# Kernel optimization log

Measured on AMD Instinct MI355X. Metric: run time of the kernel, lower is better.

Reference implementation:

```python
import jax, jax.numpy as jnp
import numpy as np

N, F, H, E, ES, G = 50000, 64, 4, 300000, 400000, 128
NS, EPS = 0.2, 1e-5  # LeakyReLU slope, BN eps


def setup_inputs() -> dict:
    k = jax.random.split(jax.random.key(0), 16)
    rn = lambda i, s, sc=1.0: jax.random.normal(k[i], s, jnp.float32) * sc
    return {
        "x": rn(0, (N, F)),
        "edge_index": jax.random.randint(k[1], (2, E), 0, N),
        "batch": jnp.sort(jax.random.randint(k[2], (N,), 0, G)),
        "scatter_edge_index": jax.random.randint(k[3], (4, 2, ES), 0, N),
        "scatter_edge_attr": rn(4, (4, ES), 0.1),
        "gat_W": rn(5, (4, F, H * F), 0.05),
        "gat_asrc": rn(6, (4, H, F), 0.05),
        "gat_adst": rn(7, (4, H, F), 0.05),
        "gat_bias": jnp.zeros((4, H * F)),
        "mlp_W": rn(8, (4, H * F, F), 0.05),
        "mlp_b": jnp.zeros((4, F)),
        "mlp_g": jnp.ones((4, F)), "mlp_beta": jnp.zeros((4, F)),
        "mlp_rm": jnp.zeros((4, F)), "mlp_rv": jax.random.uniform(k[9], (4, F)) + 0.5,
        "fc1_W": rn(10, (F, 256), 0.05), "fc1_b": jnp.zeros((256,)),
        "fc1_g": jnp.ones((256,)), "fc1_beta": jnp.zeros((256,)),
        "fc1_rm": jnp.zeros((256,)), "fc1_rv": jax.random.uniform(k[11], (256,)) + 0.5,
        "fc2_W": rn(12, (256, 64), 0.05), "fc2_b": jnp.zeros((64,)),
        "fc2_g": jnp.ones((64,)), "fc2_beta": jnp.zeros((64,)),
        "fc2_rm": jnp.zeros((64,)), "fc2_rv": jax.random.uniform(k[13], (64,)) + 0.5,
        "fc3_W": rn(14, (64, 10), 0.05), "fc3_b": jnp.zeros((10,)),
        "fc3_g": jnp.ones((10,)), "fc3_beta": jnp.zeros((10,)),
        "fc3_rm": jnp.zeros((10,)), "fc3_rv": jax.random.uniform(k[15], (10,)) + 0.5,
    }


def _bn(h, g, b, rm, rv):
    # BatchNorm1d in eval mode (running stats)
    return g * (h - rm) * jax.lax.rsqrt(rv + EPS) + b


def _forward(floats, ints):
    (x, sea, gW, gas, gad, gb, mW, mb, mg, mbe, mrm, mrv,
     f1W, f1b, f1g, f1be, f1rm, f1rv, f2W, f2b, f2g, f2be, f2rm, f2rv,
     f3W, f3b, f3g, f3be, f3rm, f3rv) = floats
    edge_index, batch, sei = ints
    n = x.shape[0]
    loop = jnp.arange(n)
    src = jnp.concatenate([edge_index[0], loop])  # GATConv adds self-loops
    dst = jnp.concatenate([edge_index[1], loop])

    def solo(i, h):
        # edge_attr-weighted scatter-add (solo_pass, aggr='add')
        s, t = sei[i, 0], sei[i, 1]
        return jax.ops.segment_sum(sea[i][:, None] * h[s], t, num_segments=n)

    def gat_mlp(i, h):
        hh = (h @ gW[i]).reshape(n, H, F)                       # [N,H,F]
        e = (hh * gas[i]).sum(-1)[src] + (hh * gad[i]).sum(-1)[dst]  # [E+N,H]
        e = jnp.where(e > 0, e, NS * e)                         # LeakyReLU(0.2)
        m = jax.ops.segment_max(e, dst, num_segments=n)         # segment softmax over dst
        ex = jnp.exp(e - m[dst])
        ssum = jax.ops.segment_sum(ex, dst, num_segments=n)
        alpha = ex / ssum[dst]
        out = jax.ops.segment_sum(hh[src] * alpha[:, :, None], dst, num_segments=n)
        out = out.reshape(n, H * F) + gb[i]                     # concat heads + bias
        h2 = jax.nn.elu(out) @ mW[i] + mb[i]                    # ELU -> Dropout(eval) -> Linear
        return _bn(h2, mg[i], mbe[i], mrm[i], mrv[i])

    x0 = solo(0, x)
    xh = [jnp.abs(solo(i, x)) for i in (1, 2, 3)]
    branches = [x0] + [solo(0, h) for h in xh]
    branches = [gat_mlp(i, branches[i]) for i in range(4)]
    x_stage2 = x + branches[0] + branches[1] + branches[2] + branches[3]
    pooled = jax.ops.segment_sum(x_stage2, batch, num_segments=G)   # global_add_pool
    h = jax.nn.relu(_bn(pooled @ f1W + f1b, f1g, f1be, f1rm, f1rv))
    h = jax.nn.relu(_bn(h @ f2W + f2b, f2g, f2be, f2rm, f2rv))
    return _bn(h @ f3W + f3b, f3g, f3be, f3rm, f3rv)  # [G, num_classes]


def reference(x, edge_index, batch, scatter_edge_index, scatter_edge_attr, gat_W, gat_asrc, gat_adst, gat_bias, mlp_W, mlp_b, mlp_g, mlp_beta, mlp_rm, mlp_rv, fc1_W, fc1_b, fc1_g, fc1_beta, fc1_rm, fc1_rv, fc2_W, fc2_b, fc2_g, fc2_beta, fc2_rm, fc2_rv, fc3_W, fc3_b, fc3_g, fc3_beta, fc3_rm, fc3_rv):
    floats = (x, scatter_edge_attr, gat_W, gat_asrc, gat_adst, gat_bias, mlp_W, mlp_b, mlp_g, mlp_beta, mlp_rm, mlp_rv, fc1_W, fc1_b, fc1_g, fc1_beta, fc1_rm, fc1_rv, fc2_W, fc2_b, fc2_g, fc2_beta, fc2_rm, fc2_rv, fc3_W, fc3_b, fc3_g, fc3_beta, fc3_rm, fc3_rv)
    return _forward(floats, (edge_index, batch, scatter_edge_index))
```

## Files before the change

kernel.cpp:

```cpp
#include <hip/hip_runtime.h>

typedef unsigned int uint;
typedef unsigned short u16;

#define NN 50000
#define FF 64
#define NHD 4
#define EE 300000
#define ESN 400000
#define NG 128
#define NSLOPE 0.2f
#define EPSBN 1e-5f

#define BINSZ 64
#define NBIN 782
#define CHUNK 2048
#define NBLK 196
#define BST 40
#define BCAP 38

typedef float f32x4 __attribute__((ext_vector_type(4)));
typedef float f32x2 __attribute__((ext_vector_type(2)));
typedef short bf16x8 __attribute__((ext_vector_type(8)));
union U8 { uint4 u; bf16x8 s; };

static __device__ __forceinline__ float lrelu(float e) {
  return fmaxf(e, NSLOPE * e);
}
static __device__ __forceinline__ float bl(uint u) {
  return __uint_as_float(u << 16);
}
static __device__ __forceinline__ float bh(uint u) {
  return __uint_as_float(u & 0xFFFF0000u);
}
static __device__ __forceinline__ uint f2bf(float f) {
  uint u = __float_as_uint(f);
  return (u + 0x7FFFu + ((u >> 16) & 1u)) >> 16;
}
static __device__ __forceinline__ uint packbf(float a, float b) {
  return f2bf(a) | (f2bf(b) << 16);
}

__global__ __launch_bounds__(256) void k_setup(
    const float2* __restrict__ x, const float* __restrict__ gW,
    const float* __restrict__ gas, const float* __restrict__ gad,
    const float* __restrict__ mW, const float* __restrict__ mb,
    const float* __restrict__ mg, const float* __restrict__ mbe,
    const float* __restrict__ mrm, const float* __restrict__ mrv,
    uint* __restrict__ xbf, uint* __restrict__ WB2, float* __restrict__ wasd,
    uint* __restrict__ MB, float* __restrict__ cvec) {
  int i = blockIdx.x * 256 + threadIdx.x;
  if (i < NN * 32) {
    float2 v = x[i];
    xbf[i] = packbf(v.x, v.y);
  }
  int t = i;
  if (t < 8192) {
    int b = t >> 11, id = t & 2047;
    int h = id >> 9, r2 = id & 511;
    int q2 = r2 >> 8, r3 = r2 & 255;
    int ct = r3 >> 6, l = r3 & 63;
    int c = h * 64 + ct * 16 + (l & 15);
    int k0 = q2 * 32 + (l >> 4) * 8;
    const float* Wp = gW + b * 16384;
    uint4 o;
    o.x = packbf(Wp[(k0 + 0) * 256 + c], Wp[(k0 + 1) * 256 + c]);
    o.y = packbf(Wp[(k0 + 2) * 256 + c], Wp[(k0 + 3) * 256 + c]);
    o.z = packbf(Wp[(k0 + 4) * 256 + c], Wp[(k0 + 5) * 256 + c]);
    o.w = packbf(Wp[(k0 + 6) * 256 + c], Wp[(k0 + 7) * 256 + c]);
    ((uint4*)WB2)[t] = o;
  } else if (t < 8192 + 2048) {
    int id = t - 8192;
    int b = id >> 9, r = id & 511;
    int sd = r >> 8, r2 = r & 255;
    int h = r2 >> 6, k = r2 & 63;
    const float* Wp = gW + b * 16384;
    const float* ap = (sd ? gad : gas) + b * 256 + h * 64;
    float acc = 0.f;
    for (int f = 0; f < 64; ++f) acc += Wp[k * 256 + h * 64 + f] * ap[f];
    wasd[((b * 2 + sd) * 4 + h) * 64 + k] = acc;
  } else if (t < 8192 + 2048 + 8192) {
    int id = t - 10240;
    int b = id >> 11, rem = id & 2047;
    int tt = rem >> 6, l = rem & 63;
    int tile = tt >> 3, q2 = tt & 7;
    int c = tile * 16 + (l & 15);
    int k0 = q2 * 32 + (l >> 4) * 8;
    const float* Mp = mW + b * 16384;
    float sc = mg[b * 64 + c] * rsqrtf(mrv[b * 64 + c] + EPSBN);
    float v[8];
#pragma unroll
    for (int j = 0; j < 8; ++j) v[j] = Mp[(k0 + j) * 64 + c] * sc;
    uint4 o;
    o.x = packbf(v[0], v[1]); o.y = packbf(v[2], v[3]);
    o.z = packbf(v[4], v[5]); o.w = packbf(v[6], v[7]);
    ((uint4*)MB)[id] = o;
  } else if (t < 8192 + 2048 + 8192 + 64) {
    int c = t - 18432;
    float acc = 0.f;
#pragma unroll
    for (int b = 0; b < 4; ++b) {
      float sc = mg[b * 64 + c] * rsqrtf(mrv[b * 64 + c] + EPSBN);
      acc += sc * (mb[b * 64 + c] - mrm[b * 64 + c]) + mbe[b * 64 + c];
    }
    cvec[c] = acc;
  }
}

__global__ __launch_bounds__(256) void k_sort1(
    const int* __restrict__ sei, const float* __restrict__ sea,
    const int* __restrict__ ei, uint2* __restrict__ sorted,
    u16* __restrict__ offs) {
  __shared__ uint hist[NBIN];
  __shared__ uint wsum[4];
  __shared__ __align__(16) uint2 buf[CHUNK];
  int y = blockIdx.y, blk = blockIdx.x, tid = threadIdx.x;
  int E = (y < 4) ? ESN : EE;
  int e0 = blk * CHUNK;
  if (e0 >= E) return;
  int ec = E - e0; if (ec > CHUNK) ec = CHUNK;
  for (int i = tid; i < NBIN; i += 256) hist[i] = 0;
  __syncthreads();
  const int* sptr; const int* tptr; const float* wptr = 0;
  if (y < 4) {
    sptr = sei + (size_t)y * 2 * ESN; tptr = sptr + ESN;
    wptr = sea + (size_t)y * ESN;
  } else {
    sptr = ei; tptr = ei + EE;
  }
  uint2 rec[8]; uint rbin[8];
#pragma unroll
  for (int k = 0; k < 8; ++k) {
    int idx = tid + k * 256;
    rbin[k] = 0xFFFFFFFFu;
    if (idx < ec) {
      int e = e0 + idx;
      int s = sptr[e], t = tptr[e];
      uint w = (y < 4) ? (f2bf(wptr[e]) << 16) : 0u;
      rec[k].x = (uint)s | ((uint)(t & 63) << 16);
      rec[k].y = w;
      rbin[k] = (uint)(t >> 6);
      atomicAdd(&hist[rbin[k]], 1u);
    }
  }
  __syncthreads();
  int t4 = tid * 4;
  uint h0 = 0, h1 = 0, h2 = 0, h3 = 0;
  if (t4 + 0 < NBIN) h0 = hist[t4 + 0];
  if (t4 + 1 < NBIN) h1 = hist[t4 + 1];
  if (t4 + 2 < NBIN) h2 = hist[t4 + 2];
  if (t4 + 3 < NBIN) h3 = hist[t4 + 3];
  uint sl = h0 + h1 + h2 + h3;
  uint pre = sl;
#pragma unroll
  for (int off = 1; off < 64; off <<= 1) {
    uint nv = __shfl_up(pre, off);
    if ((tid & 63) >= off) pre += nv;
  }
  int wid = tid >> 6;
  if ((tid & 63) == 63) wsum[wid] = pre;
  __syncthreads();
  uint wbase = 0;
#pragma unroll
  for (int w = 0; w < 4; ++w) if (w < wid) wbase += wsum[w];
  uint base = wbase + pre - sl;
  if (t4 + 0 < NBIN) hist[t4 + 0] = base;
  if (t4 + 1 < NBIN) hist[t4 + 1] = base + h0;
  if (t4 + 2 < NBIN) hist[t4 + 2] = base + h0 + h1;
  if (t4 + 3 < NBIN) hist[t4 + 3] = base + h0 + h1 + h2;
  __syncthreads();
  u16* ob = offs + ((size_t)y * NBLK + blk) * 784;
  for (int i = tid; i < NBIN; i += 256) ob[i] = (u16)hist[i];
  if (tid == 0) { ob[NBIN] = (u16)ec; ob[NBIN + 1] = (u16)ec; }
  __syncthreads();
#pragma unroll
  for (int k = 0; k < 8; ++k) {
    if (rbin[k] != 0xFFFFFFFFu) {
      uint p = atomicAdd(&hist[rbin[k]], 1u);
      buf[p] = rec[k];
    }
  }
  __syncthreads();
  uint2* sb = sorted + ((size_t)y * NBLK + blk) * CHUNK;
  uint4* s4 = (uint4*)sb;
  const uint4* b4 = (const uint4*)buf;
  int n4 = (ec + 1) >> 1;
  for (int i = tid; i < n4; i += 256) s4[i] = b4[i];
}

__global__ __launch_bounds__(256) void k_sort2(
    const u16* __restrict__ offs, const uint2* __restrict__ sorted,
    uint* __restrict__ pbk, uint* __restrict__ gbk) {
  __shared__ __align__(16) uint Lb[BINSZ * BST];
  __shared__ uint Lc[BINSZ];
  int y = blockIdx.y, bin = blockIdx.x, tid = threadIdx.x;
  if (tid < BINSZ) Lc[tid] = 0u;
  __syncthreads();
  int nblk = (y < 4) ? NBLK : 147;
  for (int sb = tid; sb < nblk; sb += 256) {
    const u16* ob = offs + ((size_t)y * NBLK + sb) * 784;
    uint st = ob[bin], en = ob[bin + 1];
    const uint2* src = sorted + ((size_t)y * NBLK + sb) * CHUNK;
    for (uint i = st; i < en; ++i) {
      uint2 r = src[i];
      uint tl = (r.x >> 16) & 63u;
      uint p = atomicAdd(&Lc[tl], 1u);
      if (p < BCAP) Lb[tl * BST + 2 + p] = (r.x & 0xFFFFu) | r.y;
    }
  }
  __syncthreads();
  if (tid < BINSZ) Lb[tid * BST] = Lc[tid];
  __syncthreads();
  int n0 = bin * BINSZ;
  int nodes = NN - n0;
  if (nodes > BINSZ) nodes = BINSZ;
  uint* out = (y < 4) ? (pbk + ((size_t)y * NN + n0) * BST)
                      : (gbk + (size_t)n0 * BST);
  int tot4 = nodes * (BST / 4);
  uint4* o4v = (uint4*)out;
  const uint4* L4 = (const uint4*)Lb;
  for (int i = tid; i < tot4; i += 256) o4v[i] = L4[i];
}

__global__ __launch_bounds__(256) void k_solo_gA(
    const uint* __restrict__ xbf, const uint* __restrict__ pbk,
    const float* __restrict__ wasd, uint* __restrict__ bbuf,
    uint* __restrict__ tmpb, float* __restrict__ es4,
    float* __restrict__ ed4) {
  int i = blockIdx.y;
  int tid = threadIdx.x;
  int n = blockIdx.x * 32 + (tid >> 3);
  int sl = tid & 7;
  if (n >= NN) return;
  const uint* bk = pbk + ((size_t)i * NN + n) * BST;
  int deg = (int)bk[0]; deg = deg > BCAP ? BCAP : deg;
  const uint* pp = bk + 2;
  f32x2 A0 = {0.f, 0.f}, A1 = {0.f, 0.f}, A2 = {0.f, 0.f}, A3 = {0.f, 0.f};
  f32x2 B0 = {0.f, 0.f}, B1 = {0.f, 0.f}, B2 = {0.f, 0.f}, B3 = {0.f, 0.f};
  for (int j = 0; j < deg; j += 2) {
    uint2 pe2 = *(const uint2*)&pp[j];
    if (j + 1 >= deg) pe2.y = 0u;
    float w0 = bh(pe2.x), w1 = bh(pe2.y);
    f32x2 w20 = {w0, w0}, w21 = {w1, w1};
    uint4 v0 = *(const uint4*)&xbf[(size_t)(pe2.x & 0xFFFFu) * 32 + sl * 4];
    uint4 v1 = *(const uint4*)&xbf[(size_t)(pe2.y & 0xFFFFu) * 32 + sl * 4];
    A0 += (f32x2){bl(v0.x), bh(v0.x)} * w20;
    A1 += (f32x2){bl(v0.y), bh(v0.y)} * w20;
    A2 += (f32x2){bl(v0.z), bh(v0.z)} * w20;
    A3 += (f32x2){bl(v0.w), bh(v0.w)} * w20;
    B0 += (f32x2){bl(v1.x), bh(v1.x)} * w21;
    B1 += (f32x2){bl(v1.y), bh(v1.y)} * w21;
    B2 += (f32x2){bl(v1.z), bh(v1.z)} * w21;
    B3 += (f32x2){bl(v1.w), bh(v1.w)} * w21;
  }
  A0 += B0; A1 += B1; A2 += B2; A3 += B3;
  uint4 o;
  o.x = packbf(A0[0], A0[1]); o.y = packbf(A1[0], A1[1]);
  o.z = packbf(A2[0], A2[1]); o.w = packbf(A3[0], A3[1]);
  uint* out = (i == 0) ? bbuf : (tmpb + (size_t)(i - 1) * NN * 32);
  *(uint4*)&out[(size_t)n * 32 + sl * 4] = o;
  if (i == 0) {
    float pv[8] = {A0[0], A0[1], A1[0], A1[1], A2[0], A2[1], A3[0], A3[1]};
    const float* wa = wasd;
    float r[8];
#pragma unroll
    for (int o8 = 0; o8 < 8; ++o8) {
      const float* w8 = wa + o8 * 64 + sl * 8;
      float a = 0.f;
#pragma unroll
      for (int j = 0; j < 8; ++j) a += pv[j] * w8[j];
      r[o8] = a;
    }
#pragma unroll
    for (int off = 1; off < 8; off <<= 1)
#pragma unroll
      for (int o8 = 0; o8 < 8; ++o8) r[o8] += __shfl_xor(r[o8], off);
    if (sl == 0) {
      *(float4*)&es4[(size_t)n * 4] = make_float4(r[0], r[1], r[2], r[3]);
      *(float4*)&ed4[(size_t)n * 4] = make_float4(r[4], r[5], r[6], r[7]);
    }
  }
}

__global__ __launch_bounds__(256) void k_solo_gB(
    const uint* __restrict__ tmpb, const uint* __restrict__ pbk,
    const float* __restrict__ wasd, uint* __restrict__ bbuf,
    float* __restrict__ es4, float* __restrict__ ed4) {
  int j0 = blockIdx.y;
  int b = j0 + 1;
  int tid = threadIdx.x;
  int n = blockIdx.x * 32 + (tid >> 3);
  int sl = tid & 7;
  if (n >= NN) return;
  const uint* bk = pbk + (size_t)n * BST;
  int deg = (int)bk[0]; deg = deg > BCAP ? BCAP : deg;
  const uint* pp = bk + 2;
  const uint* tin = tmpb + (size_t)j0 * NN * 32;
  f32x2 A0 = {0.f, 0.f}, A1 = {0.f, 0.f}, A2 = {0.f, 0.f}, A3 = {0.f, 0.f};
  f32x2 B0 = {0.f, 0.f}, B1 = {0.f, 0.f}, B2 = {0.f, 0.f}, B3 = {0.f, 0.f};
  for (int j = 0; j < deg; j += 2) {
    uint2 pe2 = *(const uint2*)&pp[j];
    if (j + 1 >= deg) pe2.y = 0u;
    float w0 = bh(pe2.x), w1 = bh(pe2.y);
    f32x2 w20 = {w0, w0}, w21 = {w1, w1};
    uint4 v0 = *(const uint4*)&tin[(size_t)(pe2.x & 0xFFFFu) * 32 + sl * 4];
    uint4 v1 = *(const uint4*)&tin[(size_t)(pe2.y & 0xFFFFu) * 32 + sl * 4];
    A0 += (f32x2){fabsf(bl(v0.x)), fabsf(bh(v0.x))} * w20;
    A1 += (f32x2){fabsf(bl(v0.y)), fabsf(bh(v0.y))} * w20;
    A2 += (f32x2){fabsf(bl(v0.z)), fabsf(bh(v0.z))} * w20;
    A3 += (f32x2){fabsf(bl(v0.w)), fabsf(bh(v0.w))} * w20;
    B0 += (f32x2){fabsf(bl(v1.x)), fabsf(bh(v1.x))} * w21;
    B1 += (f32x2){fabsf(bl(v1.y)), fabsf(bh(v1.y))} * w21;
    B2 += (f32x2){fabsf(bl(v1.z)), fabsf(bh(v1.z))} * w21;
    B3 += (f32x2){fabsf(bl(v1.w)), fabsf(bh(v1.w))} * w21;
  }
  A0 += B0; A1 += B1; A2 += B2; A3 += B3;
  uint4 o;
  o.x = packbf(A0[0], A0[1]); o.y = packbf(A1[0], A1[1]);
  o.z = packbf(A2[0], A2[1]); o.w = packbf(A3[0], A3[1]);
  *(uint4*)&bbuf[(size_t)b * NN * 32 + (size_t)n * 32 + sl * 4] = o;
  {
    float pv[8] = {A0[0], A0[1], A1[0], A1[1], A2[0], A2[1], A3[0], A3[1]};
    const float* wa = wasd + b * 512;
    float r[8];
#pragma unroll
    for (int o8 = 0; o8 < 8; ++o8) {
      const float* w8 = wa + o8 * 64 + sl * 8;
      float a = 0.f;
#pragma unroll
      for (int j = 0; j < 8; ++j) a += pv[j] * w8[j];
      r[o8] = a;
    }
#pragma unroll
    for (int off = 1; off < 8; off <<= 1)
#pragma unroll
      for (int o8 = 0; o8 < 8; ++o8) r[o8] += __shfl_xor(r[o8], off);
    if (sl == 0) {
      *(float4*)&es4[(size_t)b * NN * 4 + (size_t)n * 4] =
          make_float4(r[0], r[1], r[2], r[3]);
      *(float4*)&ed4[(size_t)b * NN * 4 + (size_t)n * 4] =
          make_float4(r[4], r[5], r[6], r[7]);
    }
  }
}

__global__ __launch_bounds__(256) void k_agg(
    const uint* __restrict__ gbk, const float* __restrict__ es4,
    const float* __restrict__ ed4, const uint* __restrict__ bbuf,
    uint* __restrict__ agg4) {
  __shared__ uint gbr[32][40];
  __shared__ uint2 meta[32][32];
  int br = blockIdx.y;
  const float4* es44 = (const float4*)(es4 + (size_t)br * NN * 4);
  const float4* ed44 = (const float4*)(ed4 + (size_t)br * NN * 4);
  const uint* bbf = bbuf + (size_t)br * NN * 32;
  int tid = threadIdx.x;
  int n0 = blockIdx.x * 32;
  for (int idx = tid; idx < 320; idx += 256) {
    int i = idx / 10, q = idx % 10;
    int nd = n0 + i;
    uint4 v = (nd < NN) ? *(const uint4*)&gbk[(size_t)nd * BST + q * 4]
                        : make_uint4(0, 0, 0, 0);
    *(uint4*)&gbr[i][q * 4] = v;
  }
  __syncthreads();
  {
    int g = tid >> 5, hl = tid & 31;
#pragma unroll
    for (int rep = 0; rep < 4; ++rep) {
      int i = rep * 8 + g;
      int nd = n0 + i;
      bool vld = nd < NN;
      int nds = vld ? nd : 0;
      int deg = vld ? (int)gbr[i][0] : 0;
      deg = deg > 31 ? 31 : deg;
      int s0 = (hl < deg) ? (int)gbr[i][2 + hl] : nds;
      bool act = hl <= deg;
      float4 edd = ed44[nds];
      float4 e4 = es44[s0];
      float val[4];
      val[0] = act ? lrelu(e4.x + edd.x) : -3e38f;
      val[1] = act ? lrelu(e4.y + edd.y) : -3e38f;
      val[2] = act ? lrelu(e4.z + edd.z) : -3e38f;
      val[3] = act ? lrelu(e4.w + edd.w) : -3e38f;
      float m[4] = {val[0], val[1], val[2], val[3]};
#pragma unroll
      for (int off = 1; off < 32; off <<= 1)
#pragma unroll
        for (int h = 0; h < 4; ++h) m[h] = fmaxf(m[h], __shfl_xor(m[h], off));
      float e[4], sm[4];
#pragma unroll
      for (int h = 0; h < 4; ++h) {
        e[h] = act ? __expf(val[h] - m[h]) : 0.f;
        sm[h] = e[h];
      }
#pragma unroll
      for (int off = 1; off < 32; off <<= 1)
#pragma unroll
        for (int h = 0; h < 4; ++h) sm[h] += __shfl_xor(sm[h], off);
      meta[i][hl] = make_uint2(packbf(e[0] / sm[0], e[1] / sm[1]),
                               packbf(e[2] / sm[2], e[3] / sm[3]));
    }
  }
  __syncthreads();
  {
    int wv = tid >> 6, l = tid & 63;
    int i = wv * 8 + (l >> 3), sl = l & 7;
    int nd = n0 + i;
    bool vld = nd < NN;
    int self = vld ? nd : 0;
    int deg = vld ? (int)gbr[i][0] : 0;
    deg = deg > 31 ? 31 : deg;
    int tot = deg + 1;
    f32x2 a00={0.f,0.f},a01={0.f,0.f},a02={0.f,0.f},a03={0.f,0.f};
    f32x2 a10={0.f,0.f},a11={0.f,0.f},a12={0.f,0.f},a13={0.f,0.f};
    f32x2 a20={0.f,0.f},a21={0.f,0.f},a22={0.f,0.f},a23={0.f,0.f};
    f32x2 a30={0.f,0.f},a31={0.f,0.f},a32={0.f,0.f},a33={0.f,0.f};
    f32x2 c00={0.f,0.f},c01={0.f,0.f},c02={0.f,0.f},c03={0.f,0.f};
    f32x2 c10={0.f,0.f},c11={0.f,0.f},c12={0.f,0.f},c13={0.f,0.f};
    f32x2 c20={0.f,0.f},c21={0.f,0.f},c22={0.f,0.f},c23={0.f,0.f};
    f32x2 c30={0.f,0.f},c31={0.f,0.f},c32={0.f,0.f},c33={0.f,0.f};
    for (int j = 0; j < tot; j += 2) {
      int j1 = j + 1;
      int src0 = (j < deg) ? (int)gbr[i][2 + j] : self;
      int src1 = (j1 < deg) ? (int)gbr[i][2 + j1] : self;
      uint2 al0 = meta[i][j];
      uint2 al1 = meta[i][j1];
      uint4 v0 = *(const uint4*)&bbf[(size_t)src0 * 32 + sl * 4];
      uint4 v1 = *(const uint4*)&bbf[(size_t)src1 * 32 + sl * 4];
      f32x2 w0={bl(al0.x),bl(al0.x)}, w1={bh(al0.x),bh(al0.x)};
      f32x2 w2={bl(al0.y),bl(al0.y)}, w3={bh(al0.y),bh(al0.y)};
      f32x2 p0={bl(v0.x),bh(v0.x)}, p1={bl(v0.y),bh(v0.y)};
      f32x2 p2={bl(v0.z),bh(v0.z)}, p3={bl(v0.w),bh(v0.w)};
      a00+=p0*w0; a01+=p1*w0; a02+=p2*w0; a03+=p3*w0;
      a10+=p0*w1; a11+=p1*w1; a12+=p2*w1; a13+=p3*w1;
      a20+=p0*w2; a21+=p1*w2; a22+=p2*w2; a23+=p3*w2;
      a30+=p0*w3; a31+=p1*w3; a32+=p2*w3; a33+=p3*w3;
      f32x2 y0={bl(al1.x),bl(al1.x)}, y1={bh(al1.x),bh(al1.x)};
      f32x2 y2={bl(al1.y),bl(al1.y)}, y3={bh(al1.y),bh(al1.y)};
      f32x2 q0={bl(v1.x),bh(v1.x)}, q1={bl(v1.y),bh(v1.y)};
      f32x2 q2={bl(v1.z),bh(v1.z)}, q3={bl(v1.w),bh(v1.w)};
      c00+=q0*y0; c01+=q1*y0; c02+=q2*y0; c03+=q3*y0;
      c10+=q0*y1; c11+=q1*y1; c12+=q2*y1; c13+=q3*y1;
      c20+=q0*y2; c21+=q1*y2; c22+=q2*y2; c23+=q3*y2;
      c30+=q0*y3; c31+=q1*y3; c32+=q2*y3; c33+=q3*y3;
    }
    a00+=c00; a01+=c01; a02+=c02; a03+=c03;
    a10+=c10; a11+=c11; a12+=c12; a13+=c13;
    a20+=c20; a21+=c21; a22+=c22; a23+=c23;
    a30+=c30; a31+=c31; a32+=c32; a33+=c33;
    if (vld) {
      uint* outp = agg4 + ((size_t)br * NN + nd) * 128;
      uint4 o;
      o.x=packbf(a00[0],a00[1]); o.y=packbf(a01[0],a01[1]);
      o.z=packbf(a02[0],a02[1]); o.w=packbf(a03[0],a03[1]);
      *(uint4*)&outp[0 * 32 + sl * 4] = o;
      o.x=packbf(a10[0],a10[1]); o.y=packbf(a11[0],a11[1]);
      o.z=packbf(a12[0],a12[1]); o.w=packbf(a13[0],a13[1]);
      *(uint4*)&outp[1 * 32 + sl * 4] = o;
      o.x=packbf(a20[0],a20[1]); o.y=packbf(a21[0],a21[1]);
      o.z=packbf(a22[0],a22[1]); o.w=packbf(a23[0],a23[1]);
      *(uint4*)&outp[2 * 32 + sl * 4] = o;
      o.x=packbf(a30[0],a30[1]); o.y=packbf(a31[0],a31[1]);
      o.z=packbf(a32[0],a32[1]); o.w=packbf(a33[0],a33[1]);
      *(uint4*)&outp[3 * 32 + sl * 4] = o;
    }
  }
}

__global__ __launch_bounds__(256) void k_mlp2(
    const uint* __restrict__ agg4, const uint* __restrict__ WB2,
    const uint* __restrict__ MB4, const float* __restrict__ gb,
    const float* __restrict__ cvec, const float* __restrict__ xsrc,
    float* __restrict__ xs2) {
  __shared__ union UU2 {
    uint elu[4][32][32];
    float red[4][32][64];
  } u;
  int tid = threadIdx.x, wv = tid >> 6, l = tid & 63;
  int quad = l >> 4, m16 = l & 15;
  int n0 = blockIdx.x * 32;
  int h = wv;
  f32x4 macc[2][4] = {{{0.f,0.f,0.f,0.f},{0.f,0.f,0.f,0.f},
                       {0.f,0.f,0.f,0.f},{0.f,0.f,0.f,0.f}},
                      {{0.f,0.f,0.f,0.f},{0.f,0.f,0.f,0.f},
                       {0.f,0.f,0.f,0.f},{0.f,0.f,0.f,0.f}}};
  u16* eluw = (u16*)&u.elu[wv][0][0];
  for (int br = 0; br < 4; ++br) {
    uint4 Bh[2][4];
#pragma unroll
    for (int kk = 0; kk < 2; ++kk)
#pragma unroll
      for (int ct = 0; ct < 4; ++ct)
        Bh[kk][ct] =
            ((const uint4*)WB2)[(((br * 4 + h) * 2 + kk) * 4 + ct) * 64 + l];
#pragma unroll
    for (int mt = 0; mt < 2; ++mt) {
      int node = n0 + mt * 16 + m16;
      const uint* ap = agg4 + ((size_t)br * NN + node) * 128 + h * 32;
      U8 a0, a1;
      a0.u = *(const uint4*)&ap[quad * 4];
      a1.u = *(const uint4*)&ap[16 + quad * 4];
#pragma unroll
      for (int ct = 0; ct < 4; ++ct) {
        f32x4 acc = {0.f, 0.f, 0.f, 0.f};
        U8 b0, b1; b0.u = Bh[0][ct]; b1.u = Bh[1][ct];
        acc = __builtin_amdgcn_mfma_f32_16x16x32_bf16(a0.s, b0.s, acc, 0, 0, 0);
        acc = __builtin_amdgcn_mfma_f32_16x16x32_bf16(a1.s, b1.s, acc, 0, 0, 0);
        float gbv = gb[br * 256 + h * 64 + ct * 16 + m16];
#pragma unroll
        for (int r = 0; r < 4; ++r) {
          float v = acc[r] + gbv;
          v = v > 0.f ? v : (__expf(v) - 1.f);
          int row = mt * 16 + quad * 4 + r;
          int ucs = ((ct * 16 + m16) >> 1) ^ ((row & 7) << 2);
          eluw[(row * 32 + ucs) * 2 + (m16 & 1)] = (u16)f2bf(v);
        }
      }
    }
    const uint4* MBb = (const uint4*)MB4 + br * 2048;
    uint4 Bm[4][2];
#pragma unroll
    for (int t = 0; t < 4; ++t)
#pragma unroll
      for (int kk = 0; kk < 2; ++kk)
        Bm[t][kk] = MBb[(t * 8 + wv * 2 + kk) * 64 + l];
#pragma unroll
    for (int mt = 0; mt < 2; ++mt) {
      int row = mt * 16 + m16;
      int sw = (row & 7) << 2;
      const uint* er = &u.elu[wv][row][0];
      U8 a0, a1;
      a0.u = *(const uint4*)&er[(quad * 4) ^ sw];
      a1.u = *(const uint4*)&er[(16 + quad * 4) ^ sw];
#pragma unroll
      for (int t = 0; t < 4; ++t) {
        U8 b0, b1; b0.u = Bm[t][0]; b1.u = Bm[t][1];
        macc[mt][t] =
            __builtin_amdgcn_mfma_f32_16x16x32_bf16(a0.s, b0.s, macc[mt][t], 0, 0, 0);
        macc[mt][t] =
            __builtin_amdgcn_mfma_f32_16x16x32_bf16(a1.s, b1.s, macc[mt][t], 0, 0, 0);
      }
    }
  }
  __syncthreads();
#pragma unroll
  for (int mt = 0; mt < 2; ++mt)
#pragma unroll
    for (int t = 0; t < 4; ++t)
#pragma unroll
      for (int r = 0; r < 4; ++r)
        u.red[wv][mt * 16 + quad * 4 + r][t * 16 + m16] = macc[mt][t][r];
  __syncthreads();
  for (int e = tid; e < 2048; e += 256) {
    int node = e >> 6, col = e & 63;
    int nd = n0 + node;
    if (nd < NN) {
      float v = u.red[0][node][col] + u.red[1][node][col] +
                u.red[2][node][col] + u.red[3][node][col];
      size_t idx = (size_t)nd * 64 + col;
      xs2[idx] = xsrc[idx] + v + cvec[col];
    }
  }
}

__global__ __launch_bounds__(256) void k_poolhead(
    const float* __restrict__ xs2, const int* __restrict__ batch,
    const float* __restrict__ f1W, const float* __restrict__ f1b,
    const float* __restrict__ f1g, const float* __restrict__ f1be,
    const float* __restrict__ f1rm, const float* __restrict__ f1rv,
    const float* __restrict__ f2W, const float* __restrict__ f2b,
    const float* __restrict__ f2g, const float* __restrict__ f2be,
    const float* __restrict__ f2rm, const float* __restrict__ f2rv,
    const float* __restrict__ f3W, const float* __restrict__ f3b,
    const float* __restrict__ f3g, const float* __restrict__ f3be,
    const float* __restrict__ f3rm, const float* __restrict__ f3rv,
    float* __restrict__ out) {
  __shared__ float p[64], h1[256], h2[64], red[4][64];
  int g = blockIdx.x, tid = threadIdx.x;
  int wv = tid >> 6, lane = tid & 63;
  int lo = 0, hi = NN;
  while (lo < hi) { int mid = (lo + hi) >> 1; if (batch[mid] < g) lo = mid + 1; else hi = mid; }
  int beg = lo;
  lo = 0; hi = NN;
  while (lo < hi) { int mid = (lo + hi) >> 1; if (batch[mid] < g + 1) lo = mid + 1; else hi = mid; }
  int end = lo;
  float acc = 0.f;
  for (int n = beg + wv; n < end; n += 4) acc += xs2[(size_t)n * FF + lane];
  red[wv][lane] = acc;
  __syncthreads();
  if (tid < 64) p[tid] = red[0][tid] + red[1][tid] + red[2][tid] + red[3][tid];
  __syncthreads();
  {
    float a = f1b[tid];
    for (int k = 0; k < 64; ++k) a += p[k] * f1W[k * 256 + tid];
    a = f1g[tid] * (a - f1rm[tid]) * rsqrtf(f1rv[tid] + EPSBN) + f1be[tid];
    h1[tid] = a > 0.f ? a : 0.f;
  }
  __syncthreads();
  if (tid < 64) {
    float b = f2b[tid];
    for (int k = 0; k < 256; ++k) b += h1[k] * f2W[k * 64 + tid];
    b = f2g[tid] * (b - f2rm[tid]) * rsqrtf(f2rv[tid] + EPSBN) + f2be[tid];
    h2[tid] = b > 0.f ? b : 0.f;
  }
  __syncthreads();
  if (tid < 10) {
    float c = f3b[tid];
    for (int k = 0; k < 64; ++k) c += h2[k] * f3W[k * 10 + tid];
    c = f3g[tid] * (c - f3rm[tid]) * rsqrtf(f3rv[tid] + EPSBN) + f3be[tid];
    out[g * 10 + tid] = c;
  }
}

extern "C" void kernel_launch(void* const* d_in, const int* in_sizes, int n_in,
                              void* d_out, int out_size, void* d_ws,
                              size_t ws_size, hipStream_t stream) {
  const float* x     = (const float*)d_in[0];
  const int*   ei    = (const int*)d_in[1];
  const int*   batch = (const int*)d_in[2];
  const int*   sei   = (const int*)d_in[3];
  const float* sea   = (const float*)d_in[4];
  const float* gW    = (const float*)d_in[5];
  const float* gas   = (const float*)d_in[6];
  const float* gad   = (const float*)d_in[7];
  const float* gb    = (const float*)d_in[8];
  const float* mW    = (const float*)d_in[9];
  const float* mb    = (const float*)d_in[10];
  const float* mg    = (const float*)d_in[11];
  const float* mbe   = (const float*)d_in[12];
  const float* mrm   = (const float*)d_in[13];
  const float* mrv   = (const float*)d_in[14];
  const float* f1W   = (const float*)d_in[15];
  const float* f1b   = (const float*)d_in[16];
  const float* f1g   = (const float*)d_in[17];
  const float* f1be  = (const float*)d_in[18];
  const float* f1rm  = (const float*)d_in[19];
  const float* f1rv  = (const float*)d_in[20];
  const float* f2W   = (const float*)d_in[21];
  const float* f2b   = (const float*)d_in[22];
  const float* f2g   = (const float*)d_in[23];
  const float* f2be  = (const float*)d_in[24];
  const float* f2rm  = (const float*)d_in[25];
  const float* f2rv  = (const float*)d_in[26];
  const float* f3W   = (const float*)d_in[27];
  const float* f3b   = (const float*)d_in[28];
  const float* f3g   = (const float*)d_in[29];
  const float* f3be  = (const float*)d_in[30];
  const float* f3rm  = (const float*)d_in[31];
  const float* f3rv  = (const float*)d_in[32];
  float* out = (float*)d_out;

  char* base = (char*)d_ws;
  float* xs2 = (float*)base;
  uint* gbk  = (uint*)(base + (size_t)NN * 64 * 4);
  uint* xbf  = gbk + (size_t)NN * BST;
  uint* bbuf = xbf + (size_t)NN * 32;
  uint* tmpb = bbuf + (size_t)4 * NN * 32;
  uint* pbk  = tmpb + (size_t)3 * NN * 32;
  uint2* sorted = (uint2*)(pbk + (size_t)4 * NN * BST);
  u16* offs = (u16*)(sorted + (size_t)5 * NBLK * CHUNK);
  uint* agg4 = (uint*)(offs + (size_t)5 * NBLK * 784);
  float* es4 = (float*)(agg4 + ((size_t)4 * NN + 32) * 128);
  float* ed4 = es4 + (size_t)4 * NN * 4;
  float* cvec = ed4 + (size_t)4 * NN * 4;
  float* wasd = cvec + 64;
  uint* WB2 = (uint*)(wasd + 2048);
  uint* MB4 = WB2 + 4 * 8192;

  size_t need = (size_t)((char*)(MB4 + 4 * 8192) - base);
  if (ws_size < need) return;

  k_setup<<<(NN * 32 + 255) / 256, 256, 0, stream>>>(
      (const float2*)x, gW, gas, gad, mW, mb, mg, mbe, mrm, mrv, xbf, WB2,
      wasd, MB4, cvec);

  dim3 gS1(NBLK, 5);
  k_sort1<<<gS1, 256, 0, stream>>>(sei, sea, ei, sorted, offs);
  dim3 gS2(NBIN, 5);
  k_sort2<<<gS2, 256, 0, stream>>>(offs, sorted, pbk, gbk);

  dim3 gA((NN + 31) / 32, 4);
  k_solo_gA<<<gA, 256, 0, stream>>>(xbf, pbk, wasd, bbuf, tmpb, es4, ed4);
  dim3 gB((NN + 31) / 32, 3);
  k_solo_gB<<<gB, 256, 0, stream>>>(tmpb, pbk, wasd, bbuf, es4, ed4);

  dim3 gAg((NN + 31) / 32, 4);
  k_agg<<<gAg, 256, 0, stream>>>(gbk, es4, ed4, bbuf, agg4);
  k_mlp2<<<(NN + 31) / 32, 256, 0, stream>>>(agg4, WB2, MB4, gb, cvec, x, xs2);

  k_poolhead<<<NG, 256, 0, stream>>>(xs2, batch, f1W, f1b, f1g, f1be, f1rm,
                                     f1rv, f2W, f2b, f2g, f2be, f2rm, f2rv,
                                     f3W, f3b, f3g, f3be, f3rm, f3rv, out);
}
```

Baseline: 427.8 us.

## Sort nodes by degree within bins and fuse three solo_gB branches per thread

k_sort2 now orders the 64 nodes of each bin by descending in-degree and stores the node id in each bucket record. The solo and aggregation kernels walk these permuted positions and scatter results by id, so neighbouring threads see similar trip counts and warp divergence drops. k_solo_gB also handles all three branches in one thread, loading each edge record once and issuing three gathers per edge instead of launching three grid rows. This costs a small shared-memory prefix sum and permuted, less coalesced output writes, and the fused kernel holds more registers.

```diff
diff --git a/kernel.cpp b/kernel.cpp
--- a/kernel.cpp
+++ b/kernel.cpp
@@ -14,6 +14,7 @@
 
 #define BINSZ 64
 #define NBIN 782
+#define NPOS (NBIN * BINSZ)
 #define CHUNK 2048
 #define NBLK 196
 #define BST 40
@@ -193,8 +194,10 @@
     uint* __restrict__ pbk, uint* __restrict__ gbk) {
   __shared__ __align__(16) uint Lb[BINSZ * BST];
   __shared__ uint Lc[BINSZ];
+  __shared__ uint dh[64], dpos[64], sperm[64];
   int y = blockIdx.y, bin = blockIdx.x, tid = threadIdx.x;
   if (tid < BINSZ) Lc[tid] = 0u;
+  if (tid < 64) dh[tid] = 0u;
   __syncthreads();
   int nblk = (y < 4) ? NBLK : 147;
   for (int sb = tid; sb < nblk; sb += 256) {
@@ -209,17 +212,38 @@
     }
   }
   __syncthreads();
-  if (tid < BINSZ) Lb[tid * BST] = Lc[tid];
-  __syncthreads();
-  int n0 = bin * BINSZ;
-  int nodes = NN - n0;
-  if (nodes > BINSZ) nodes = BINSZ;
-  uint* out = (y < 4) ? (pbk + ((size_t)y * NN + n0) * BST)
-                      : (gbk + (size_t)n0 * BST);
-  int tot4 = nodes * (BST / 4);
+  uint myd = 0;
+  if (tid < 64) {
+    myd = Lc[tid]; if (myd > 63u) myd = 63u;
+    atomicAdd(&dh[63u - myd], 1u);
+  }
+  __syncthreads();
+  if (tid < 64) {
+    uint v = dh[tid], p = v;
+#pragma unroll
+    for (int off = 1; off < 64; off <<= 1) {
+      uint nv = __shfl_up(p, off);
+      if (tid >= off) p += nv;
+    }
+    dpos[tid] = p - v;
+  }
+  __syncthreads();
+  if (tid < 64) {
+    uint slot = atomicAdd(&dpos[63u - myd], 1u);
+    sperm[slot] = (uint)tid;
+    Lb[tid * BST + 0] = Lc[tid];
+    Lb[tid * BST + 1] = (uint)(bin * BINSZ + tid);
+  }
+  __syncthreads();
+  uint* out = (y < 4) ? (pbk + ((size_t)y * NPOS + (size_t)bin * BINSZ) * BST)
+                      : (gbk + (size_t)bin * BINSZ * BST);
   uint4* o4v = (uint4*)out;
-  const uint4* L4 = (const uint4*)Lb;
-  for (int i = tid; i < tot4; i += 256) o4v[i] = L4[i];
+  for (int i = tid; i < 64 * (BST / 4); i += 256) {
+    int pos = i / (BST / 4), q = i % (BST / 4);
+    uint sn = sperm[pos];
+    uint4 v = *(const uint4*)&Lb[sn * BST + q * 4];
+    o4v[(size_t)pos * (BST / 4) + q] = v;
+  }
 }
 
 __global__ __launch_bounds__(256) void k_solo_gA(
@@ -229,11 +253,12 @@
     float* __restrict__ ed4) {
   int i = blockIdx.y;
   int tid = threadIdx.x;
-  int n = blockIdx.x * 32 + (tid >> 3);
+  int pos = blockIdx.x * 32 + (tid >> 3);
   int sl = tid & 7;
-  if (n >= NN) return;
-  const uint* bk = pbk + ((size_t)i * NN + n) * BST;
+  const uint* bk = pbk + ((size_t)i * NPOS + pos) * BST;
   int deg = (int)bk[0]; deg = deg > BCAP ? BCAP : deg;
+  int id = (int)bk[1];
+  if (id >= NN) return;
   const uint* pp = bk + 2;
   f32x2 A0 = {0.f, 0.f}, A1 = {0.f, 0.f}, A2 = {0.f, 0.f}, A3 = {0.f, 0.f};
   f32x2 B0 = {0.f, 0.f}, B1 = {0.f, 0.f}, B2 = {0.f, 0.f}, B3 = {0.f, 0.f};
@@ -258,7 +283,7 @@
   o.x = packbf(A0[0], A0[1]); o.y = packbf(A1[0], A1[1]);
   o.z = packbf(A2[0], A2[1]); o.w = packbf(A3[0], A3[1]);
   uint* out = (i == 0) ? bbuf : (tmpb + (size_t)(i - 1) * NN * 32);
-  *(uint4*)&out[(size_t)n * 32 + sl * 4] = o;
+  *(uint4*)&out[(size_t)id * 32 + sl * 4] = o;
   if (i == 0) {
     float pv[8] = {A0[0], A0[1], A1[0], A1[1], A2[0], A2[1], A3[0], A3[1]};
     const float* wa = wasd;
@@ -276,8 +301,8 @@
 #pragma unroll
       for (int o8 = 0; o8 < 8; ++o8) r[o8] += __shfl_xor(r[o8], off);
     if (sl == 0) {
-      *(float4*)&es4[(size_t)n * 4] = make_float4(r[0], r[1], r[2], r[3]);
-      *(float4*)&ed4[(size_t)n * 4] = make_float4(r[4], r[5], r[6], r[7]);
+      *(float4*)&es4[(size_t)id * 4] = make_float4(r[0], r[1], r[2], r[3]);
+      *(float4*)&ed4[(size_t)id * 4] = make_float4(r[4], r[5], r[6], r[7]);
     }
   }
 }
@@ -286,41 +311,52 @@
     const uint* __restrict__ tmpb, const uint* __restrict__ pbk,
     const float* __restrict__ wasd, uint* __restrict__ bbuf,
     float* __restrict__ es4, float* __restrict__ ed4) {
-  int j0 = blockIdx.y;
-  int b = j0 + 1;
   int tid = threadIdx.x;
-  int n = blockIdx.x * 32 + (tid >> 3);
+  int pos = blockIdx.x * 32 + (tid >> 3);
   int sl = tid & 7;
-  if (n >= NN) return;
-  const uint* bk = pbk + (size_t)n * BST;
+  const uint* bk = pbk + (size_t)pos * BST;
   int deg = (int)bk[0]; deg = deg > BCAP ? BCAP : deg;
+  int id = (int)bk[1];
+  if (id >= NN) return;
   const uint* pp = bk + 2;
-  const uint* tin = tmpb + (size_t)j0 * NN * 32;
-  f32x2 A0 = {0.f, 0.f}, A1 = {0.f, 0.f}, A2 = {0.f, 0.f}, A3 = {0.f, 0.f};
-  f32x2 B0 = {0.f, 0.f}, B1 = {0.f, 0.f}, B2 = {0.f, 0.f}, B3 = {0.f, 0.f};
-  for (int j = 0; j < deg; j += 2) {
-    uint2 pe2 = *(const uint2*)&pp[j];
-    if (j + 1 >= deg) pe2.y = 0u;
-    float w0 = bh(pe2.x), w1 = bh(pe2.y);
-    f32x2 w20 = {w0, w0}, w21 = {w1, w1};
-    uint4 v0 = *(const uint4*)&tin[(size_t)(pe2.x & 0xFFFFu) * 32 + sl * 4];
-    uint4 v1 = *(const uint4*)&tin[(size_t)(pe2.y & 0xFFFFu) * 32 + sl * 4];
-    A0 += (f32x2){fabsf(bl(v0.x)), fabsf(bh(v0.x))} * w20;
-    A1 += (f32x2){fabsf(bl(v0.y)), fabsf(bh(v0.y))} * w20;
-    A2 += (f32x2){fabsf(bl(v0.z)), fabsf(bh(v0.z))} * w20;
-    A3 += (f32x2){fabsf(bl(v0.w)), fabsf(bh(v0.w))} * w20;
-    B0 += (f32x2){fabsf(bl(v1.x)), fabsf(bh(v1.x))} * w21;
-    B1 += (f32x2){fabsf(bl(v1.y)), fabsf(bh(v1.y))} * w21;
-    B2 += (f32x2){fabsf(bl(v1.z)), fabsf(bh(v1.z))} * w21;
-    B3 += (f32x2){fabsf(bl(v1.w)), fabsf(bh(v1.w))} * w21;
-  }
-  A0 += B0; A1 += B1; A2 += B2; A3 += B3;
-  uint4 o;
-  o.x = packbf(A0[0], A0[1]); o.y = packbf(A1[0], A1[1]);
-  o.z = packbf(A2[0], A2[1]); o.w = packbf(A3[0], A3[1]);
-  *(uint4*)&bbuf[(size_t)b * NN * 32 + (size_t)n * 32 + sl * 4] = o;
-  {
-    float pv[8] = {A0[0], A0[1], A1[0], A1[1], A2[0], A2[1], A3[0], A3[1]};
+  const uint* t0 = tmpb;
+  const uint* t1 = tmpb + (size_t)NN * 32;
+  const uint* t2 = tmpb + (size_t)2 * NN * 32;
+  f32x2 A[3][4];
+#pragma unroll
+  for (int k = 0; k < 3; ++k)
+#pragma unroll
+    for (int c = 0; c < 4; ++c) A[k][c] = (f32x2){0.f, 0.f};
+  for (int j = 0; j < deg; ++j) {
+    uint pe = pp[j];
+    float w = bh(pe);
+    f32x2 w2 = {w, w};
+    size_t ro = (size_t)(pe & 0xFFFFu) * 32 + sl * 4;
+    uint4 v0 = *(const uint4*)&t0[ro];
+    uint4 v1 = *(const uint4*)&t1[ro];
+    uint4 v2 = *(const uint4*)&t2[ro];
+    A[0][0] += (f32x2){fabsf(bl(v0.x)), fabsf(bh(v0.x))} * w2;
+    A[0][1] += (f32x2){fabsf(bl(v0.y)), fabsf(bh(v0.y))} * w2;
+    A[0][2] += (f32x2){fabsf(bl(v0.z)), fabsf(bh(v0.z))} * w2;
+    A[0][3] += (f32x2){fabsf(bl(v0.w)), fabsf(bh(v0.w))} * w2;
+    A[1][0] += (f32x2){fabsf(bl(v1.x)), fabsf(bh(v1.x))} * w2;
+    A[1][1] += (f32x2){fabsf(bl(v1.y)), fabsf(bh(v1.y))} * w2;
+    A[1][2] += (f32x2){fabsf(bl(v1.z)), fabsf(bh(v1.z))} * w2;
+    A[1][3] += (f32x2){fabsf(bl(v1.w)), fabsf(bh(v1.w))} * w2;
+    A[2][0] += (f32x2){fabsf(bl(v2.x)), fabsf(bh(v2.x))} * w2;
+    A[2][1] += (f32x2){fabsf(bl(v2.y)), fabsf(bh(v2.y))} * w2;
+    A[2][2] += (f32x2){fabsf(bl(v2.z)), fabsf(bh(v2.z))} * w2;
+    A[2][3] += (f32x2){fabsf(bl(v2.w)), fabsf(bh(v2.w))} * w2;
+  }
+#pragma unroll
+  for (int k = 0; k < 3; ++k) {
+    int b = k + 1;
+    uint4 o;
+    o.x = packbf(A[k][0][0], A[k][0][1]); o.y = packbf(A[k][1][0], A[k][1][1]);
+    o.z = packbf(A[k][2][0], A[k][2][1]); o.w = packbf(A[k][3][0], A[k][3][1]);
+    *(uint4*)&bbuf[(size_t)b * NN * 32 + (size_t)id * 32 + sl * 4] = o;
+    float pv[8] = {A[k][0][0], A[k][0][1], A[k][1][0], A[k][1][1],
+                   A[k][2][0], A[k][2][1], A[k][3][0], A[k][3][1]};
     const float* wa = wasd + b * 512;
     float r[8];
 #pragma unroll
@@ -336,9 +372,9 @@
 #pragma unroll
       for (int o8 = 0; o8 < 8; ++o8) r[o8] += __shfl_xor(r[o8], off);
     if (sl == 0) {
-      *(float4*)&es4[(size_t)b * NN * 4 + (size_t)n * 4] =
+      *(float4*)&es4[(size_t)b * NN * 4 + (size_t)id * 4] =
           make_float4(r[0], r[1], r[2], r[3]);
-      *(float4*)&ed4[(size_t)b * NN * 4 + (size_t)n * 4] =
+      *(float4*)&ed4[(size_t)b * NN * 4 + (size_t)id * 4] =
           make_float4(r[4], r[5], r[6], r[7]);
     }
   }
@@ -355,13 +391,11 @@
   const float4* ed44 = (const float4*)(ed4 + (size_t)br * NN * 4);
   const uint* bbf = bbuf + (size_t)br * NN * 32;
   int tid = threadIdx.x;
-  int n0 = blockIdx.x * 32;
+  int p0 = blockIdx.x * 32;
   for (int idx = tid; idx < 320; idx += 256) {
     int i = idx / 10, q = idx % 10;
-    int nd = n0 + i;
-    uint4 v = (nd < NN) ? *(const uint4*)&gbk[(size_t)nd * BST + q * 4]
-                        : make_uint4(0, 0, 0, 0);
-    *(uint4*)&gbr[i][q * 4] = v;
+    *(uint4*)&gbr[i][q * 4] =
+        *(const uint4*)&gbk[((size_t)p0 + i) * BST + q * 4];
   }
   __syncthreads();
   {
@@ -369,9 +403,9 @@
 #pragma unroll
     for (int rep = 0; rep < 4; ++rep) {
       int i = rep * 8 + g;
-      int nd = n0 + i;
-      bool vld = nd < NN;
-      int nds = vld ? nd : 0;
+      int id = (int)gbr[i][1];
+      bool vld = id < NN;
+      int nds = vld ? id : 0;
       int deg = vld ? (int)gbr[i][0] : 0;
       deg = deg > 31 ? 31 : deg;
       int s0 = (hl < deg) ? (int)gbr[i][2 + hl] : nds;
@@ -406,9 +440,9 @@
   {
     int wv = tid >> 6, l = tid & 63;
     int i = wv * 8 + (l >> 3), sl = l & 7;
-    int nd = n0 + i;
-    bool vld = nd < NN;
-    int self = vld ? nd : 0;
+    int id = (int)gbr[i][1];
+    bool vld = id < NN;
+    int self = vld ? id : 0;
     int deg = vld ? (int)gbr[i][0] : 0;
     deg = deg > 31 ? 31 : deg;
     int tot = deg + 1;
@@ -430,12 +464,12 @@
       uint4 v1 = *(const uint4*)&bbf[(size_t)src1 * 32 + sl * 4];
       f32x2 w0={bl(al0.x),bl(al0.x)}, w1={bh(al0.x),bh(al0.x)};
       f32x2 w2={bl(al0.y),bl(al0.y)}, w3={bh(al0.y),bh(al0.y)};
-      f32x2 p0={bl(v0.x),bh(v0.x)}, p1={bl(v0.y),bh(v0.y)};
-      f32x2 p2={bl(v0.z),bh(v0.z)}, p3={bl(v0.w),bh(v0.w)};
-      a00+=p0*w0; a01+=p1*w0; a02+=p2*w0; a03+=p3*w0;
-      a10+=p0*w1; a11+=p1*w1; a12+=p2*w1; a13+=p3*w1;
-      a20+=p0*w2; a21+=p1*w2; a22+=p2*w2; a23+=p3*w2;
-      a30+=p0*w3; a31+=p1*w3; a32+=p2*w3; a33+=p3*w3;
+      f32x2 p0_={bl(v0.x),bh(v0.x)}, p1_={bl(v0.y),bh(v0.y)};
+      f32x2 p2_={bl(v0.z),bh(v0.z)}, p3_={bl(v0.w),bh(v0.w)};
+      a00+=p0_*w0; a01+=p1_*w0; a02+=p2_*w0; a03+=p3_*w0;
+      a10+=p0_*w1; a11+=p1_*w1; a12+=p2_*w1; a13+=p3_*w1;
+      a20+=p0_*w2; a21+=p1_*w2; a22+=p2_*w2; a23+=p3_*w2;
+      a30+=p0_*w3; a31+=p1_*w3; a32+=p2_*w3; a33+=p3_*w3;
       f32x2 y0={bl(al1.x),bl(al1.x)}, y1={bh(al1.x),bh(al1.x)};
       f32x2 y2={bl(al1.y),bl(al1.y)}, y3={bh(al1.y),bh(al1.y)};
       f32x2 q0={bl(v1.x),bh(v1.x)}, q1={bl(v1.y),bh(v1.y)};
@@ -450,7 +484,7 @@
     a20+=c20; a21+=c21; a22+=c22; a23+=c23;
     a30+=c30; a31+=c31; a32+=c32; a33+=c33;
     if (vld) {
-      uint* outp = agg4 + ((size_t)br * NN + nd) * 128;
+      uint* outp = agg4 + ((size_t)br * NN + id) * 128;
       uint4 o;
       o.x=packbf(a00[0],a00[1]); o.y=packbf(a01[0],a01[1]);
       o.z=packbf(a02[0],a02[1]); o.w=packbf(a03[0],a03[1]);
@@ -654,11 +688,11 @@
   char* base = (char*)d_ws;
   float* xs2 = (float*)base;
   uint* gbk  = (uint*)(base + (size_t)NN * 64 * 4);
-  uint* xbf  = gbk + (size_t)NN * BST;
+  uint* xbf  = gbk + (size_t)NPOS * BST;
   uint* bbuf = xbf + (size_t)NN * 32;
   uint* tmpb = bbuf + (size_t)4 * NN * 32;
   uint* pbk  = tmpb + (size_t)3 * NN * 32;
-  uint2* sorted = (uint2*)(pbk + (size_t)4 * NN * BST);
+  uint2* sorted = (uint2*)(pbk + (size_t)4 * NPOS * BST);
   u16* offs = (u16*)(sorted + (size_t)5 * NBLK * CHUNK);
   uint* agg4 = (uint*)(offs + (size_t)5 * NBLK * 784);
   float* es4 = (float*)(agg4 + ((size_t)4 * NN + 32) * 128);
@@ -680,12 +714,11 @@
   dim3 gS2(NBIN, 5);
   k_sort2<<<gS2, 256, 0, stream>>>(offs, sorted, pbk, gbk);
 
-  dim3 gA((NN + 31) / 32, 4);
+  dim3 gA(NPOS / 32, 4);
   k_solo_gA<<<gA, 256, 0, stream>>>(xbf, pbk, wasd, bbuf, tmpb, es4, ed4);
-  dim3 gB((NN + 31) / 32, 3);
-  k_solo_gB<<<gB, 256, 0, stream>>>(tmpb, pbk, wasd, bbuf, es4, ed4);
-
-  dim3 gAg((NN + 31) / 32, 4);
+  k_solo_gB<<<NPOS / 32, 256, 0, stream>>>(tmpb, pbk, wasd, bbuf, es4, ed4);
+
+  dim3 gAg(NPOS / 32, 4);
   k_agg<<<gAg, 256, 0, stream>>>(gbk, es4, ed4, bbuf, agg4);
   k_mlp2<<<(NN + 31) / 32, 256, 0, stream>>>(agg4, WB2, MB4, gb, cvec, x, xs2);
 
```

Result: no change. 426.7 us (-0.3%).
